# Kernel optimization log

Measured on AMD Instinct MI355X. Metric: run time of the kernel, lower is better.

Reference implementation:

```python
import jax, jax.numpy as jnp
import numpy as np

B, N, C = 64, 320, 768
H = 12
D = C // H  # 64 head dim


def setup_inputs() -> dict:
    key = jax.random.key(0)
    k1, k2, k3, k4, k5 = jax.random.split(key, 5)
    s = 0.02
    return {
        "x": jax.random.normal(k1, (B, N, C), jnp.float32),
        "w_qkv": jax.random.normal(k2, (3 * C, C), jnp.float32) * s,
        "b_qkv": jax.random.normal(k3, (3 * C,), jnp.float32) * s,
        "w_proj": jax.random.normal(k4, (C, C), jnp.float32) * s,
        "b_proj": jax.random.normal(k5, (C,), jnp.float32) * s,
        "num_t": 64,
        "num_s": 256,
    }


def reference(x, w_qkv, b_qkv, w_proj, b_proj, num_t, num_s):
    Bx, Nx, Cx = x.shape
    scale = 1.0 / jnp.sqrt(jnp.asarray(D, x.dtype))
    # qkv projection: [B,N,3C] -> [3,B,H,N,D]
    qkv = x @ w_qkv.T + b_qkv
    qkv = qkv.reshape(Bx, Nx, 3, H, D).transpose(2, 0, 3, 1, 4)
    q, k, v = qkv[0], qkv[1], qkv[2]
    q_t, q_s = q[:, :, :num_t], q[:, :, num_t:]
    k_t = k[:, :, :num_t]
    v_t = v[:, :, :num_t]
    # template self-attention: [B,H,num_t,num_t]
    attn_t = jax.nn.softmax(jnp.einsum("bhqd,bhkd->bhqk", q_t, k_t) * scale, axis=-1)
    x_t = jnp.einsum("bhqk,bhkd->bhqd", attn_t, v_t)
    x_t = x_t.transpose(0, 2, 1, 3).reshape(Bx, num_t, Cx)
    # search attends to all tokens: [B,H,num_s,N]
    attn_s = jax.nn.softmax(jnp.einsum("bhqd,bhkd->bhqk", q_s, k) * scale, axis=-1)
    x_s = jnp.einsum("bhqk,bhkd->bhqd", attn_s, v)
    x_s = x_s.transpose(0, 2, 1, 3).reshape(Bx, num_s, Cx)
    out = jnp.concatenate([x_t, x_s], axis=1)
    return out @ w_proj.T + b_proj
```

## Files before the change

kernel.cpp:

```cpp
#include <hip/hip_runtime.h>
#include <hip/hip_bf16.h>


typedef __attribute__((ext_vector_type(8))) short short8;
typedef __attribute__((ext_vector_type(4))) float f32x4;
typedef __hip_bfloat16 bf16;

#define NTOK 320
#define CDIM 768
#define NHEAD 12
#define MFMA16(a,b,c) __builtin_amdgcn_mfma_f32_16x16x32_bf16((a),(b),(c),0,0,0)

__device__ __forceinline__ unsigned short bfbits(float v) {
    bf16 h = __float2bfloat16(v);
    unsigned short u; __builtin_memcpy(&u, &h, 2);
    return u;
}

__device__ __forceinline__ short8 ldfrag(const bf16* p) { return *(const short8*)p; }
__device__ __forceinline__ short8 ldfrag(const float* p) {
    float4 a = *(const float4*)p;
    float4 b = *(const float4*)(p + 4);
    short8 r;
    r[0]=(short)bfbits(a.x); r[1]=(short)bfbits(a.y); r[2]=(short)bfbits(a.z); r[3]=(short)bfbits(a.w);
    r[4]=(short)bfbits(b.x); r[5]=(short)bfbits(b.y); r[6]=(short)bfbits(b.z); r[7]=(short)bfbits(b.w);
    return r;
}

__device__ __forceinline__ void stage16(const bf16* g, bf16* l) {
    __builtin_amdgcn_global_load_lds(
        (const __attribute__((address_space(1))) void*)g,
        (__attribute__((address_space(3))) void*)l, 16, 0, 0);
}

__global__ __launch_bounds__(256) void cvt3_kernel(const float* __restrict__ s0, bf16* __restrict__ d0, int n0,
                                                   const float* __restrict__ s1, bf16* __restrict__ d1, int n1,
                                                   const float* __restrict__ s2, bf16* __restrict__ d2, int n2)
{
    const int ntot = n0 + n1 + n2;
    int i = blockIdx.x * 256 + threadIdx.x;
    const int stride = gridDim.x * 256;
    for (; i < ntot; i += stride) {
        const float* s; bf16* d; int j = i;
        if (j < n0)              { s = s0; d = d0; }
        else if ((j -= n0) < n1) { s = s1; d = d1; }
        else                     { j -= n1; s = s2; d = d2; }
        const float4 a = ((const float4*)s)[2 * (size_t)j];
        const float4 b = ((const float4*)s)[2 * (size_t)j + 1];
        short8 r;
        r[0]=(short)bfbits(a.x); r[1]=(short)bfbits(a.y); r[2]=(short)bfbits(a.z); r[3]=(short)bfbits(a.w);
        r[4]=(short)bfbits(b.x); r[5]=(short)bfbits(b.y); r[6]=(short)bfbits(b.z); r[7]=(short)bfbits(b.w);
        ((short8*)d)[j] = r;
    }
}

template<int NOUT, int EPI, int BF16B>
__global__ __launch_bounds__(256) void gemm_bt16(const bf16* __restrict__ A,
                                                 const void* __restrict__ Bmv,
                                                 const float* __restrict__ bias,
                                                 void* __restrict__ o0,
                                                 void* __restrict__ o1,
                                                 void* __restrict__ o2)
{
    __shared__ alignas(16) bf16 As[128 * 32];
    __shared__ alignas(16) bf16 Bs[128 * 32];
    const int tid  = threadIdx.x;
    const int lane = tid & 63;
    const int wv   = tid >> 6;
    const int r16  = lane & 15;
    const int kg   = lane >> 4;

    constexpr int GX  = NOUT / 128;
    constexpr int NWG = GX * 160;
    int flat = blockIdx.y * GX + blockIdx.x;
    flat = (flat & 7) * (NWG >> 3) + (flat >> 3);
    const int byy = flat / GX;
    const int bxx = flat - byy * GX;
    const int m0  = byy * 128;
    const int n0  = bxx * 128;
    const int wm  = (wv & 1) * 64;
    const int wn  = (wv >> 1) * 64;

    const bf16*  Ab   = A + (size_t)m0 * CDIM;
    const bf16*  Bb16 = (const bf16*)Bmv  + (size_t)n0 * CDIM;
    const float* Bb32 = (const float*)Bmv + (size_t)n0 * CDIM;

    const int ra0 = tid >> 2;
    const int ca0 = (tid & 3) * 8;

    bf16* lA0 = &As[(size_t)(wv * 64) * 8];
    bf16* lA1 = &As[(size_t)(wv * 64 + 256) * 8];
    bf16* lB0 = &Bs[(size_t)(wv * 64) * 8];
    bf16* lB1 = &Bs[(size_t)(wv * 64 + 256) * 8];

    f32x4 acc[4][4] = {};

    for (int k0 = 0; k0 < CDIM; k0 += 32) {
        if constexpr (BF16B) {
            __syncthreads();
            stage16(Ab   + (size_t)ra0        * CDIM + k0 + ca0, lA0);
            stage16(Ab   + (size_t)(ra0 + 64) * CDIM + k0 + ca0, lA1);
            stage16(Bb16 + (size_t)ra0        * CDIM + k0 + ca0, lB0);
            stage16(Bb16 + (size_t)(ra0 + 64) * CDIM + k0 + ca0, lB1);
            __syncthreads();
        } else {
            short8 gb0 = ldfrag(Bb32 + (size_t)ra0        * CDIM + k0 + ca0);
            short8 gb1 = ldfrag(Bb32 + (size_t)(ra0 + 64) * CDIM + k0 + ca0);
            __syncthreads();
            stage16(Ab + (size_t)ra0        * CDIM + k0 + ca0, lA0);
            stage16(Ab + (size_t)(ra0 + 64) * CDIM + k0 + ca0, lA1);
            *(short8*)&Bs[(size_t)tid * 8]         = gb0;
            *(short8*)&Bs[(size_t)(tid + 256) * 8] = gb1;
            __syncthreads();
        }

        short8 af[4], bfr[4];
        #pragma unroll
        for (int mt = 0; mt < 4; mt++)
            af[mt] = *(const short8*)&As[(wm + mt * 16 + r16) * 32 + kg * 8];
        #pragma unroll
        for (int nt = 0; nt < 4; nt++)
            bfr[nt] = *(const short8*)&Bs[(wn + nt * 16 + r16) * 32 + kg * 8];
        #pragma unroll
        for (int mt = 0; mt < 4; mt++)
            #pragma unroll
            for (int nt = 0; nt < 4; nt++)
                acc[mt][nt] = MFMA16(af[mt], bfr[nt], acc[mt][nt]);
    }

    #pragma unroll
    for (int nt = 0; nt < 4; nt++) {
        const int gn = n0 + wn + nt * 16 + r16;
        const float bv = bias[gn];
        if (EPI == 0) {
            const int which = gn / CDIM;
            const int rem   = gn - which * CDIM;
            const int hh    = rem >> 6;
            const int dd    = rem & 63;
            #pragma unroll
            for (int mt = 0; mt < 4; mt++) {
                const int gm0  = m0 + wm + mt * 16 + kg * 4;
                const int bidx = gm0 / NTOK;
                const int nn0  = gm0 - bidx * NTOK;
                float v[4];
                #pragma unroll
                for (int r = 0; r < 4; r++) v[r] = acc[mt][nt][r] + bv;
                if (which == 0) {
                    bf16* q = (bf16*)o0 + ((size_t)(bidx * NHEAD + hh) * NTOK + nn0) * 64 + dd;
                    #pragma unroll
                    for (int r = 0; r < 4; r++) q[(size_t)r * 64] = __float2bfloat16(v[r]);
                } else if (which == 1) {
                    bf16* k = (bf16*)o1 + ((size_t)(bidx * NHEAD + hh) * NTOK + nn0) * 64 + dd;
                    #pragma unroll
                    for (int r = 0; r < 4; r++) k[(size_t)r * 64] = __float2bfloat16(v[r]);
                } else {
                    ushort4 p;
                    unsigned short* ps = (unsigned short*)&p;
                    #pragma unroll
                    for (int r = 0; r < 4; r++) ps[r] = bfbits(v[r]);
                    *(ushort4*)((bf16*)o2 + ((size_t)(bidx * NHEAD + hh) * 64 + dd) * NTOK + nn0) = p;
                }
            }
        } else {
            float* out = (float*)o0;
            #pragma unroll
            for (int mt = 0; mt < 4; mt++) {
                const int gm0 = m0 + wm + mt * 16 + kg * 4;
                #pragma unroll
                for (int r = 0; r < 4; r++)
                    out[(size_t)(gm0 + r) * NOUT + gn] = acc[mt][nt][r] + bv;
            }
        }
    }
}

#define ATTN_NWG (768 * 10)
__global__ __launch_bounds__(256, 4) void attn_kernel(const bf16* __restrict__ q_ws,
                                                      const bf16* __restrict__ k_ws,
                                                      const bf16* __restrict__ vt_ws,
                                                      bf16* __restrict__ attn,
                                                      const int* __restrict__ numt_p)
{
    __shared__ alignas(16) float S[32 * 320];
    int num_t = 64;
    if (numt_p) {
        int v = *numt_p;
        float f = __int_as_float(v);
        if (v >= 1 && v <= 319) num_t = v;
        else if (f >= 1.f && f <= 319.f) num_t = (int)f;
    }
    if (num_t <= 0 || num_t > NTOK || (num_t & 31)) num_t = 64;

    const int tid  = threadIdx.x;
    const int lane = tid & 63;
    const int w    = tid >> 6;
    const int r16  = lane & 15;
    const int kg   = lane >> 4;

    int blk = blockIdx.x;
    blk = (blk & 7) * (ATTN_NWG / 8) + (blk >> 3);
    const int bh  = blk / 10;
    const int qt  = blk - bh * 10;
    const int b   = bh / NHEAD;
    const int h   = bh - b * NHEAD;
    const int q0  = qt * 32;
    const int nk  = (q0 + 32 <= num_t) ? num_t : NTOK;
    const int nk16 = nk >> 4;

    const bf16* qp = q_ws  + (size_t)bh * NTOK * 64;
    const bf16* kp = k_ws  + (size_t)bh * NTOK * 64;
    const bf16* vp = vt_ws + (size_t)bh * 64 * NTOK;

    short8 qf[2][2];
    #pragma unroll
    for (int ks = 0; ks < 2; ks++)
        #pragma unroll
        for (int mt = 0; mt < 2; mt++)
            qf[ks][mt] = ldfrag(qp + (size_t)(q0 + mt * 16 + r16) * 64 + ks * 32 + kg * 8);

    const float scale = 0.125f;
    auto p1body = [&](int nt) {
        f32x4 a0 = {}, a1 = {};
        #pragma unroll
        for (int ks = 0; ks < 2; ks++) {
            short8 kf = ldfrag(kp + (size_t)(nt * 16 + r16) * 64 + ks * 32 + kg * 8);
            a0 = MFMA16(qf[ks][0], kf, a0);
            a1 = MFMA16(qf[ks][1], kf, a1);
        }
        const int col = nt * 16 + r16;
        #pragma unroll
        for (int r = 0; r < 4; r++) {
            const int ro  = kg * 4 + r;
            const int swz = (ro & 7) << 2;
            S[ro * 320        + (col ^ swz)] = a0[r] * scale;
            S[(16 + ro) * 320 + (col ^ swz)] = a1[r] * scale;
        }
    };
    if (nk16 == 20) {
        #pragma unroll
        for (int it = 0; it < 5; it++) p1body(w + it * 4);
    } else {
        for (int nt = w; nt < nk16; nt += 4) p1body(nt);
    }
    __syncthreads();

    {
        const int row = tid >> 3;
        const int sub = tid & 7;
        const int swzw = (row & 7) << 2;
        const int swzh = (row & 7) << 3;
        float* Sr = S + row * 320;
        bf16*  Pr = (bf16*)Sr;
        float mx = -1e30f;
        for (int c = sub * 4; c < nk; c += 32) {
            float4 t = *(float4*)&Sr[c ^ swzw];
            mx = fmaxf(mx, fmaxf(fmaxf(t.x, t.y), fmaxf(t.z, t.w)));
        }
        #pragma unroll
        for (int m = 1; m < 8; m <<= 1) mx = fmaxf(mx, __shfl_xor(mx, m));
        float sum = 0.f;
        for (int c = sub * 4; c < nk; c += 32) {
            float4 t = *(float4*)&Sr[c ^ swzw];
            t.x = __expf(t.x - mx); t.y = __expf(t.y - mx);
            t.z = __expf(t.z - mx); t.w = __expf(t.w - mx);
            sum += t.x + t.y + t.z + t.w;
            ushort4 p;
            p.x = bfbits(t.x); p.y = bfbits(t.y); p.z = bfbits(t.z); p.w = bfbits(t.w);
            *(ushort4*)&Pr[c ^ swzh] = p;
        }
        #pragma unroll
        for (int m = 1; m < 8; m <<= 1) sum += __shfl_xor(sum, m);
        if (sub == 0) Sr[316 ^ swzw] = 1.0f / sum;
    }
    __syncthreads();

    const int mt  = w & 1;
    const int ntb = w >> 1;
    const int prow = mt * 16 + r16;
    const bf16* Pbr = (const bf16*)(S + prow * 320);
    const int pswzh = (prow & 7) << 3;
    f32x4 o[2] = {};
    auto p3body = [&](int ks) {
        short8 af = *(const short8*)&Pbr[(ks * 32 + kg * 8) ^ pswzh];
        #pragma unroll
        for (int i = 0; i < 2; i++) {
            const int nt = ntb + i * 2;
            short8 vf = ldfrag(vp + (size_t)(nt * 16 + r16) * NTOK + ks * 32 + kg * 8);
            o[i] = MFMA16(af, vf, o[i]);
        }
    };
    if (nk == NTOK) {
        #pragma unroll
        for (int ks = 0; ks < 10; ks++) p3body(ks);
    } else {
        for (int ks = 0; ks < (nk >> 5); ks++) p3body(ks);
    }
    #pragma unroll
    for (int i = 0; i < 2; i++) {
        const int nt = ntb + i * 2;
        const int dd = nt * 16 + r16;
        #pragma unroll
        for (int r = 0; r < 4; r++) {
            const int qrow  = mt * 16 + kg * 4 + r;
            const float invs = S[qrow * 320 + (316 ^ ((qrow & 7) << 2))];
            const float val = o[i][r] * invs;
            const int token = q0 + qrow;
            attn[(((size_t)b * NTOK + token) * NHEAD + h) * 64 + dd] = __float2bfloat16(val);
        }
    }
}

extern "C" void kernel_launch(void* const* d_in, const int* in_sizes, int n_in,
                              void* d_out, int out_size, void* d_ws, size_t ws_size,
                              hipStream_t stream)
{
    float* out = (float*)d_out;

    const float *x = nullptr, *w_qkv = nullptr, *b_qkv = nullptr,
                *w_proj = nullptr, *b_proj = nullptr;
    const int* numt_p = nullptr;
    for (int i = 0; i < n_in; i++) {
        switch (in_sizes[i]) {
            case 15728640: x      = (const float*)d_in[i]; break;
            case 1769472:  w_qkv  = (const float*)d_in[i]; break;
            case 2304:     b_qkv  = (const float*)d_in[i]; break;
            case 589824:   w_proj = (const float*)d_in[i]; break;
            case 768:      b_proj = (const float*)d_in[i]; break;
            case 1:        if (!numt_p) numt_p = (const int*)d_in[i]; break;
            default: break;
        }
    }
    if (!x || !w_qkv || !b_qkv || !w_proj || !b_proj) return;

    const size_t per      = (size_t)64 * NHEAD * NTOK * 64;
    const size_t wq_elems = (size_t)2304 * 768;
    const size_t wp_elems = (size_t)768 * 768;
    const size_t base_need = 4 * per * sizeof(bf16);
    const size_t full_need = base_need + (wq_elems + wp_elems) * sizeof(bf16);
    if (ws_size < base_need) return;
    const bool full = ws_size >= full_need;

    bf16* q_ws  = (bf16*)d_ws;
    bf16* k_ws  = q_ws  + per;
    bf16* vt_ws = k_ws  + per;
    bf16* attn  = vt_ws + per;
    bf16* x16   = attn;
    bf16* wq16  = attn + per;
    bf16* wp16  = wq16 + wq_elems;

    if (full)
        cvt3_kernel<<<2048, 256, 0, stream>>>(x, x16, (int)(per / 8),
                                              w_qkv, wq16, (int)(wq_elems / 8),
                                              w_proj, wp16, (int)(wp_elems / 8));
    else
        cvt3_kernel<<<2048, 256, 0, stream>>>(x, x16, (int)(per / 8),
                                              x, x16, 0, x, x16, 0);

    if (full)
        gemm_bt16<2304, 0, 1><<<dim3(18, 160), 256, 0, stream>>>(
            x16, wq16, b_qkv, q_ws, k_ws, vt_ws);
    else
        gemm_bt16<2304, 0, 0><<<dim3(18, 160), 256, 0, stream>>>(
            x16, w_qkv, b_qkv, q_ws, k_ws, vt_ws);

    attn_kernel<<<ATTN_NWG, 256, 0, stream>>>(q_ws, k_ws, vt_ws, attn, numt_p);

    if (full)
        gemm_bt16<768, 1, 1><<<dim3(6, 160), 256, 0, stream>>>(
            attn, wp16, b_proj, out, nullptr, nullptr);
    else
        gemm_bt16<768, 1, 0><<<dim3(6, 160), 256, 0, stream>>>(
            attn, w_proj, b_proj, out, nullptr, nullptr);
}
```

Measured before the change: 382.2 us.

## Double-buffer LDS tiles in bf16 GEMM path to overlap staging with MFMA

In the bf16-weight GEMM path, the shared-memory A and B tiles are doubled into two buffers. The K loop is unrolled by two so the next 32-wide K slice is staged into one buffer while MFMAs run on the other. This removes one barrier per K step and hides global-to-LDS load latency behind compute. In exchange, LDS use per workgroup doubles, which may reduce occupancy. The fp32-weight path keeps its single-buffer loop.

```diff
diff --git a/kernel.cpp b/kernel.cpp
--- a/kernel.cpp
+++ b/kernel.cpp
@@ -62,8 +62,8 @@
                                                  void* __restrict__ o1,
                                                  void* __restrict__ o2)
 {
-    __shared__ alignas(16) bf16 As[128 * 32];
-    __shared__ alignas(16) bf16 Bs[128 * 32];
+    __shared__ alignas(16) bf16 As[2 * 128 * 32];
+    __shared__ alignas(16) bf16 Bs[2 * 128 * 32];
     const int tid  = threadIdx.x;
     const int lane = tid & 63;
     const int wv   = tid >> 6;
@@ -88,44 +88,71 @@
     const int ra0 = tid >> 2;
     const int ca0 = (tid & 3) * 8;
 
-    bf16* lA0 = &As[(size_t)(wv * 64) * 8];
-    bf16* lA1 = &As[(size_t)(wv * 64 + 256) * 8];
-    bf16* lB0 = &Bs[(size_t)(wv * 64) * 8];
-    bf16* lB1 = &Bs[(size_t)(wv * 64 + 256) * 8];
-
     f32x4 acc[4][4] = {};
 
-    for (int k0 = 0; k0 < CDIM; k0 += 32) {
-        if constexpr (BF16B) {
+    if constexpr (BF16B) {
+        const bf16* gA0 = Ab   + (size_t)ra0        * CDIM + ca0;
+        const bf16* gA1 = Ab   + (size_t)(ra0 + 64) * CDIM + ca0;
+        const bf16* gB0 = Bb16 + (size_t)ra0        * CDIM + ca0;
+        const bf16* gB1 = Bb16 + (size_t)(ra0 + 64) * CDIM + ca0;
+
+        auto stage = [&](int k0, int buf) {
+            const int lb = buf * 4096;
+            stage16(gA0 + k0, &As[lb + (size_t)(wv * 64) * 8]);
+            stage16(gA1 + k0, &As[lb + (size_t)(wv * 64 + 256) * 8]);
+            stage16(gB0 + k0, &Bs[lb + (size_t)(wv * 64) * 8]);
+            stage16(gB1 + k0, &Bs[lb + (size_t)(wv * 64 + 256) * 8]);
+        };
+        auto compute = [&](int buf) {
+            const int lb = buf * 4096;
+            short8 af[4], bfr[4];
+            #pragma unroll
+            for (int mt = 0; mt < 4; mt++)
+                af[mt] = *(const short8*)&As[lb + (wm + mt * 16 + r16) * 32 + kg * 8];
+            #pragma unroll
+            for (int nt = 0; nt < 4; nt++)
+                bfr[nt] = *(const short8*)&Bs[lb + (wn + nt * 16 + r16) * 32 + kg * 8];
+            #pragma unroll
+            for (int mt = 0; mt < 4; mt++)
+                #pragma unroll
+                for (int nt = 0; nt < 4; nt++)
+                    acc[mt][nt] = MFMA16(af[mt], bfr[nt], acc[mt][nt]);
+        };
+
+        stage(0, 0);
+        __syncthreads();
+        for (int k0 = 0; k0 < CDIM; k0 += 64) {
+            stage(k0 + 32, 1);
+            compute(0);
             __syncthreads();
-            stage16(Ab   + (size_t)ra0        * CDIM + k0 + ca0, lA0);
-            stage16(Ab   + (size_t)(ra0 + 64) * CDIM + k0 + ca0, lA1);
-            stage16(Bb16 + (size_t)ra0        * CDIM + k0 + ca0, lB0);
-            stage16(Bb16 + (size_t)(ra0 + 64) * CDIM + k0 + ca0, lB1);
+            if (k0 + 64 < CDIM) stage(k0 + 64, 0);
+            compute(1);
             __syncthreads();
-        } else {
+        }
+    } else {
+        for (int k0 = 0; k0 < CDIM; k0 += 32) {
             short8 gb0 = ldfrag(Bb32 + (size_t)ra0        * CDIM + k0 + ca0);
             short8 gb1 = ldfrag(Bb32 + (size_t)(ra0 + 64) * CDIM + k0 + ca0);
             __syncthreads();
-            stage16(Ab + (size_t)ra0        * CDIM + k0 + ca0, lA0);
-            stage16(Ab + (size_t)(ra0 + 64) * CDIM + k0 + ca0, lA1);
+            stage16(Ab + (size_t)ra0        * CDIM + k0 + ca0, &As[(size_t)(wv * 64) * 8]);
+            stage16(Ab + (size_t)(ra0 + 64) * CDIM + k0 + ca0, &As[(size_t)(wv * 64 + 256) * 8]);
             *(short8*)&Bs[(size_t)tid * 8]         = gb0;
             *(short8*)&Bs[(size_t)(tid + 256) * 8] = gb1;
             __syncthreads();
-        }
-
-        short8 af[4], bfr[4];
-        #pragma unroll
-        for (int mt = 0; mt < 4; mt++)
-            af[mt] = *(const short8*)&As[(wm + mt * 16 + r16) * 32 + kg * 8];
-        #pragma unroll
-        for (int nt = 0; nt < 4; nt++)
-            bfr[nt] = *(const short8*)&Bs[(wn + nt * 16 + r16) * 32 + kg * 8];
-        #pragma unroll
-        for (int mt = 0; mt < 4; mt++)
+
+            short8 af[4], bfr[4];
+            #pragma unroll
+            for (int mt = 0; mt < 4; mt++)
+                af[mt] = *(const short8*)&As[(wm + mt * 16 + r16) * 32 + kg * 8];
             #pragma unroll
             for (int nt = 0; nt < 4; nt++)
-                acc[mt][nt] = MFMA16(af[mt], bfr[nt], acc[mt][nt]);
+                bfr[nt] = *(const short8*)&Bs[(wn + nt * 16 + r16) * 32 + kg * 8];
+            #pragma unroll
+            for (int mt = 0; mt < 4; mt++)
+                #pragma unroll
+                for (int nt = 0; nt < 4; nt++)
+                    acc[mt][nt] = MFMA16(af[mt], bfr[nt], acc[mt][nt]);
+        }
     }
 
     #pragma unroll
```

After: 389.0 us. About the same (+1.8%).

## Add 256x256 double-buffered bf16 MFMA GEMM kernel for the QKV projection

Applied to the files above, without the earlier changes.

Adds a dedicated QKV projection kernel with 256x256 output tiles, 512 threads and BK=64. It uses double-buffered, XOR-swizzled LDS staging with explicit vmcnt waits and s_setprio around the MFMA blocks. The epilogue scatters results into the head-split q/k/transposed-v layouts. The larger tile is meant to raise operand reuse and cut global traffic per FLOP relative to the 128x128 kernel. In exchange it needs 128KB of LDS and 128 accumulator floats per thread, which limits occupancy and gives fewer workgroups (720) to fill the CUs.

```diff
diff --git a/kernel.cpp b/kernel.cpp
--- a/kernel.cpp
+++ b/kernel.cpp
@@ -54,13 +54,130 @@
     }
 }
 
+__global__ __launch_bounds__(512, 2) void gemm256_k1(const bf16* __restrict__ A,
+                                                     const bf16* __restrict__ Bm,
+                                                     const float* __restrict__ bias,
+                                                     void* __restrict__ o0,
+                                                     void* __restrict__ o1,
+                                                     void* __restrict__ o2)
+{
+    __shared__ alignas(16) bf16 As[2][256 * 64];
+    __shared__ alignas(16) bf16 Bs[2][256 * 64];
+    const int tid    = threadIdx.x;
+    const int lane   = tid & 63;
+    const int wv     = tid >> 6;
+    const int r16    = lane & 15;
+    const int kg     = lane >> 4;
+    const int warp_m = wv >> 2;
+    const int warp_n = wv & 3;
+
+    constexpr int GX  = 2304 / 256;
+    constexpr int GY  = 20480 / 256;
+    constexpr int NWG = GX * GY;
+    int flat = blockIdx.y * GX + blockIdx.x;
+    flat = (flat & 7) * (NWG / 8) + (flat >> 3);
+    const int byy = flat / GX;
+    const int bxx = flat - byy * GX;
+    const int m0  = byy * 256;
+    const int n0  = bxx * 256;
+
+    const int srl  = wv * 8 + (lane >> 3);
+    const int gcol = ((lane & 7) ^ (lane >> 3)) * 8;
+    const bf16* gA = A  + (size_t)(m0 + srl) * CDIM + gcol;
+    const bf16* gB = Bm + (size_t)(n0 + srl) * CDIM + gcol;
+    const int ldsb = wv * 512;
+
+    auto stageTile = [&](int kt, int buf) {
+        const int k0 = kt * 64;
+        #pragma unroll
+        for (int j = 0; j < 4; j++)
+            stage16(gA + (size_t)j * 64 * CDIM + k0, &As[buf][j * 4096 + ldsb]);
+        #pragma unroll
+        for (int j = 0; j < 4; j++)
+            stage16(gB + (size_t)j * 64 * CDIM + k0, &Bs[buf][j * 4096 + ldsb]);
+    };
+
+    const int arow = warp_m * 128 + r16;
+    const int brow = warp_n * 64  + r16;
+    const int csw0 = ((0 * 4 + kg) ^ (r16 & 7)) * 8;
+    const int csw1 = ((1 * 4 + kg) ^ (r16 & 7)) * 8;
+
+    f32x4 acc[8][4] = {};
+
+    constexpr int NKT = CDIM / 64;
+    stageTile(0, 0);
+    stageTile(1, 1);
+    for (int kt = 0; kt < NKT; ++kt) {
+        const int buf = kt & 1;
+        if (kt < NKT - 1) { asm volatile("s_waitcnt vmcnt(8)" ::: "memory"); }
+        else              { asm volatile("s_waitcnt vmcnt(0)" ::: "memory"); }
+        __builtin_amdgcn_s_barrier();
+        asm volatile("" ::: "memory");
+        #pragma unroll
+        for (int ks = 0; ks < 2; ks++) {
+            const int csw = ks ? csw1 : csw0;
+            short8 af[8], bfm[4];
+            #pragma unroll
+            for (int m = 0; m < 8; m++)
+                af[m] = *(const short8*)&As[buf][(arow + m * 16) * 64 + csw];
+            #pragma unroll
+            for (int n = 0; n < 4; n++)
+                bfm[n] = *(const short8*)&Bs[buf][(brow + n * 16) * 64 + csw];
+            __builtin_amdgcn_s_setprio(1);
+            #pragma unroll
+            for (int m = 0; m < 8; m++)
+                #pragma unroll
+                for (int n = 0; n < 4; n++)
+                    acc[m][n] = MFMA16(af[m], bfm[n], acc[m][n]);
+            __builtin_amdgcn_s_setprio(0);
+        }
+        asm volatile("s_waitcnt lgkmcnt(0)" ::: "memory");
+        __builtin_amdgcn_s_barrier();
+        if (kt + 2 < NKT) stageTile(kt + 2, buf);
+    }
+
+    #pragma unroll
+    for (int n = 0; n < 4; n++) {
+        const int gn = n0 + warp_n * 64 + n * 16 + r16;
+        const float bv = bias[gn];
+        const int which = gn / CDIM;
+        const int rem   = gn - which * CDIM;
+        const int hh    = rem >> 6;
+        const int dd    = rem & 63;
+        #pragma unroll
+        for (int m = 0; m < 8; m++) {
+            const int gm0  = m0 + warp_m * 128 + m * 16 + kg * 4;
+            const int bidx = gm0 / NTOK;
+            const int nn0  = gm0 - bidx * NTOK;
+            float v[4];
+            #pragma unroll
+            for (int r = 0; r < 4; r++) v[r] = acc[m][n][r] + bv;
+            if (which == 0) {
+                bf16* q = (bf16*)o0 + ((size_t)(bidx * NHEAD + hh) * NTOK + nn0) * 64 + dd;
+                #pragma unroll
+                for (int r = 0; r < 4; r++) q[(size_t)r * 64] = __float2bfloat16(v[r]);
+            } else if (which == 1) {
+                bf16* k = (bf16*)o1 + ((size_t)(bidx * NHEAD + hh) * NTOK + nn0) * 64 + dd;
+                #pragma unroll
+                for (int r = 0; r < 4; r++) k[(size_t)r * 64] = __float2bfloat16(v[r]);
+            } else {
+                ushort4 p;
+                unsigned short* ps = (unsigned short*)&p;
+                #pragma unroll
+                for (int r = 0; r < 4; r++) ps[r] = bfbits(v[r]);
+                *(ushort4*)((bf16*)o2 + ((size_t)(bidx * NHEAD + hh) * 64 + dd) * NTOK + nn0) = p;
+            }
+        }
+    }
+}
+
 template<int NOUT, int EPI, int BF16B>
-__global__ __launch_bounds__(256) void gemm_bt16(const bf16* __restrict__ A,
-                                                 const void* __restrict__ Bmv,
-                                                 const float* __restrict__ bias,
-                                                 void* __restrict__ o0,
-                                                 void* __restrict__ o1,
-                                                 void* __restrict__ o2)
+__global__ __launch_bounds__(256) void gemm_bt16_s(const bf16* __restrict__ A,
+                                                   const void* __restrict__ Bmv,
+                                                   const float* __restrict__ bias,
+                                                   void* __restrict__ o0,
+                                                   void* __restrict__ o1,
+                                                   void* __restrict__ o2)
 {
     __shared__ alignas(16) bf16 As[128 * 32];
     __shared__ alignas(16) bf16 Bs[128 * 32];
@@ -357,18 +474,18 @@
                                               x, x16, 0, x, x16, 0);
 
     if (full)
-        gemm_bt16<2304, 0, 1><<<dim3(18, 160), 256, 0, stream>>>(
+        gemm256_k1<<<dim3(9, 80), 512, 0, stream>>>(
             x16, wq16, b_qkv, q_ws, k_ws, vt_ws);
     else
-        gemm_bt16<2304, 0, 0><<<dim3(18, 160), 256, 0, stream>>>(
+        gemm_bt16_s<2304, 0, 0><<<dim3(18, 160), 256, 0, stream>>>(
             x16, w_qkv, b_qkv, q_ws, k_ws, vt_ws);
 
     attn_kernel<<<ATTN_NWG, 256, 0, stream>>>(q_ws, k_ws, vt_ws, attn, numt_p);
 
     if (full)
-        gemm_bt16<768, 1, 1><<<dim3(6, 160), 256, 0, stream>>>(
+        gemm_bt16_s<768, 1, 1><<<dim3(6, 160), 256, 0, stream>>>(
             attn, wp16, b_proj, out, nullptr, nullptr);
     else
-        gemm_bt16<768, 1, 0><<<dim3(6, 160), 256, 0, stream>>>(
+        gemm_bt16_s<768, 1, 0><<<dim3(6, 160), 256, 0, stream>>>(
             attn, w_proj, b_proj, out, nullptr, nullptr);
 }
```

New measurement: 377.8 us. No clear change (-1.1%).
